# Optimization experiments

Hardware: AMD Instinct MI355X
Metric: run time of the kernel (lower is better)

Reference implementation:

```python
import jax, jax.numpy as jnp
import numpy as np

N, D_IN, F = 65536, 512, 256
E = 524288
BATCH, K1 = 32, 200
BN_EPS = 1e-5


def setup_inputs() -> dict:
    key = jax.random.key(0)
    ks = iter(jax.random.split(key, 64))

    def nrm(shape, s=0.05):
        return jax.random.normal(next(ks), shape, jnp.float32) * s

    inp = {
        "feat": jax.random.normal(next(ks), (N, D_IN), jnp.float32),
        "A": jax.random.randint(next(ks), (2, E), 0, N, dtype=jnp.int32),
        "h1id": jax.random.randint(next(ks), (BATCH * K1,), 0, N // BATCH, dtype=jnp.int32),
        "batch": BATCH,
    }
    dims = [(D_IN, F), (F, F), (F, F), (F, F)]
    for i, (di, do) in enumerate(dims, 1):
        inp[f"eps{i}"] = jnp.zeros((), jnp.float32)          # GINConv train_eps, init 0
        inp[f"w{i}a"] = nrm((di, do)); inp[f"b{i}a"] = jnp.zeros((do,), jnp.float32)
        inp[f"w{i}b"] = nrm((do, do)); inp[f"b{i}b"] = jnp.zeros((do,), jnp.float32)
        inp[f"g{i}"] = jnp.ones((do,), jnp.float32)          # BN gamma
        inp[f"be{i}"] = jnp.zeros((do,), jnp.float32)        # BN beta
        inp[f"m{i}"] = nrm((do,))                            # BN running mean
        inp[f"v{i}"] = jax.random.uniform(next(ks), (do,), jnp.float32, 0.5, 1.5)  # BN running var
    inp["wc1"] = nrm((F, F)); inp["bc1"] = jnp.zeros((F,), jnp.float32)
    inp["pa"] = jnp.full((F,), 0.25, jnp.float32)            # PReLU per-channel slope
    inp["wc2"] = nrm((F, 2)); inp["bc2"] = jnp.zeros((2,), jnp.float32)
    return inp


def _gin_conv(x, src, dst, eps, wa, ba, wb, bb, g, be, m, v):
    # sum aggregation over in-edges: aggr[i] = sum_{(j->i)} x[j]
    aggr = jax.ops.segment_sum(x[src], dst, num_segments=N)
    h = (1.0 + eps) * x + aggr
    h = jax.nn.relu(h @ wa + ba) @ wb + bb
    # BatchNorm1d in eval mode (running stats)
    return (h - m) * jax.lax.rsqrt(v + BN_EPS) * g + be


def _forward(feat, A, h1id, batch,
             eps1, w1a, b1a, w1b, b1b, g1, be1, m1, v1,
             eps2, w2a, b2a, w2b, b2b, g2, be2, m2, v2,
             eps3, w3a, b3a, w3b, b3b, g3, be3, m3, v3,
             eps4, w4a, b4a, w4b, b4b, g4, be4, m4, v4,
             wc1, bc1, pa, wc2, bc2):
    src, dst = A[0], A[1]
    h = jax.nn.relu(_gin_conv(feat, src, dst, eps1, w1a, b1a, w1b, b1b, g1, be1, m1, v1))
    h = jax.nn.relu(_gin_conv(h, src, dst, eps2, w2a, b2a, w2b, b2b, g2, be2, m2, v2))
    h = jax.nn.relu(_gin_conv(h, src, dst, eps3, w3a, b3a, w3b, b3b, g3, be3, m3, v3))
    h = _gin_conv(h, src, dst, eps4, w4a, b4a, w4b, b4b, g4, be4, m4, v4)
    score = h.reshape(batch, -1, F)                      # [B, n_per_graph, F]
    idx = h1id.reshape(batch, K1)
    edge_feat = jnp.take_along_axis(score, idx[:, :, None], axis=1)  # [B, K1, F]
    ef = edge_feat.reshape(-1, F)
    hc = ef @ wc1 + bc1
    hc = jnp.where(hc > 0, hc, pa * hc)                  # PReLU(256)
    return hc @ wc2 + bc2                                # [B*K1, 2]


def reference(feat, A, h1id, batch,
              eps1, w1a, b1a, w1b, b1b, g1, be1, m1, v1,
              eps2, w2a, b2a, w2b, b2b, g2, be2, m2, v2,
              eps3, w3a, b3a, w3b, b3b, g3, be3, m3, v3,
              eps4, w4a, b4a, w4b, b4b, g4, be4, m4, v4,
              wc1, bc1, pa, wc2, bc2):
    return _forward(feat, A, h1id, batch,
                    eps1, w1a, b1a, w1b, b1b, g1, be1, m1, v1,
                    eps2, w2a, b2a, w2b, b2b, g2, be2, m2, v2,
                    eps3, w3a, b3a, w3b, b3b, g3, be3, m3, v3,
                    eps4, w4a, b4a, w4b, b4b, g4, be4, m4, v4,
                    wc1, bc1, pa, wc2, bc2)
```

## Files before the change

kernel.cpp:

```cpp
#include <hip/hip_runtime.h>

typedef unsigned short u16;
typedef unsigned int   u32;
typedef __bf16  bf16x8 __attribute__((ext_vector_type(8)));
typedef float   f32x4  __attribute__((ext_vector_type(4)));

#define NN 65536
#define NE 524288
#define FD 256

typedef const __attribute__((address_space(1))) void* gas_p;
typedef __attribute__((address_space(3))) void* las_p;
#define GLDS16(g, l) __builtin_amdgcn_global_load_lds((gas_p)(const void*)(g), (las_p)(void*)(l), 16, 0, 0)

__device__ __forceinline__ u16 f2bf(float f){
  u32 u = __float_as_uint(f);
  u += 0x7fffu + ((u >> 16) & 1u);
  return (u16)(u >> 16);
}
__device__ __forceinline__ float bf2f(u32 lo16){
  return __uint_as_float(lo16 << 16);
}

__global__ __launch_bounds__(256) void prep_k(
    const float* __restrict__ w1a, const float* __restrict__ w1b,
    const float* __restrict__ w2a, const float* __restrict__ w2b,
    const float* __restrict__ w3a, const float* __restrict__ w3b,
    const float* __restrict__ w4a, const float* __restrict__ w4b,
    const float* __restrict__ wc1, u16* __restrict__ wT)
{
  int idx = blockIdx.x * 256 + threadIdx.x;
  const float* src; int base, K, local;
  if (idx < 131072){ src = w1a; base = 0; K = 512; local = idx; }
  else {
    local = idx - 131072;
    int j = local >> 16;
    local &= 65535;
    K = 256;
    base = 131072 + j * 65536;
    switch (j){
      case 0: src = w1b; break;
      case 1: src = w2a; break;
      case 2: src = w2b; break;
      case 3: src = w3a; break;
      case 4: src = w3b; break;
      case 5: src = w4a; break;
      case 6: src = w4b; break;
      default: src = wc1; break;
    }
  }
  int n = local & 255;
  int k = local >> 8;
  wT[base + n * K + k] = f2bf(src[k * 256 + n]);
}

__global__ __launch_bounds__(256) void hist_k(const int* __restrict__ dst, int* __restrict__ deg){
  int e = blockIdx.x * 256 + threadIdx.x;
  atomicAdd(&deg[dst[e]], 1);
}

__global__ __launch_bounds__(1024) void scan_k(const int* __restrict__ deg, int* __restrict__ rs){
  __shared__ int part[1024];
  int t = threadIdx.x;
  int base = t * 64;
  int sum = 0;
  for (int i = 0; i < 64; ++i) sum += deg[base + i];
  part[t] = sum;
  __syncthreads();
  for (int off = 1; off < 1024; off <<= 1){
    int v = 0;
    if (t >= off) v = part[t - off];
    __syncthreads();
    part[t] += v;
    __syncthreads();
  }
  int run = part[t] - sum;
  for (int i = 0; i < 64; ++i){ rs[base + i] = run; run += deg[base + i]; }
  if (t == 1023) rs[65536] = part[1023];
}

__global__ __launch_bounds__(256) void scat_k(
    const int* __restrict__ src, const int* __restrict__ dst,
    const int* __restrict__ rs, int* __restrict__ cursor, int* __restrict__ csr)
{
  int e = blockIdx.x * 256 + threadIdx.x;
  int d = dst[e];
  int pos = atomicAdd(&cursor[d], 1);
  csr[rs[d] + pos] = src[e];
}

template<int AF32, int MODE, int RELU, int K>
__global__ __launch_bounds__(256) void gemm_k(
    const void* __restrict__ Ap, const u16* __restrict__ Bt,
    u16* __restrict__ C,
    const float* __restrict__ p0, const float* __restrict__ p1,
    const float* __restrict__ p2, const float* __restrict__ p3,
    const float* __restrict__ p4)
{
  __shared__ u16 lds[128 * 136];
  u16* As = lds;
  u16* Bs = lds + 8192;
  const int t    = threadIdx.x;
  const int lane = t & 63;
  const int w    = t >> 6;
  const int wm   = w & 1;
  const int wn   = w >> 1;
  const int m0   = blockIdx.x * 128;
  const int n0   = blockIdx.y * 128;
  const int mrow = lane & 15;
  const int quad = lane >> 4;

  f32x4 acc[4][4];
  const f32x4 zero = {0.f, 0.f, 0.f, 0.f};
  #pragma unroll
  for (int i = 0; i < 4; ++i)
    #pragma unroll
    for (int j = 0; j < 4; ++j) acc[i][j] = zero;

  const u16* Ab = (const u16*)Ap;
  const float* Af = (const float*)Ap;

  for (int k0 = 0; k0 < K; k0 += 64){
    if (AF32){
      #pragma unroll
      for (int i = 0; i < 4; ++i){
        int p   = i * 256 + t;
        int row = p >> 3;
        int ch  = (p & 7) ^ (row & 7);
        const float* s = Af + (size_t)(m0 + row) * K + k0 + ch * 8;
        float4 x0 = *(const float4*)s;
        float4 x1 = *(const float4*)(s + 4);
        union { uint4 q; u16 h[8]; } u;
        u.h[0] = f2bf(x0.x); u.h[1] = f2bf(x0.y); u.h[2] = f2bf(x0.z); u.h[3] = f2bf(x0.w);
        u.h[4] = f2bf(x1.x); u.h[5] = f2bf(x1.y); u.h[6] = f2bf(x1.z); u.h[7] = f2bf(x1.w);
        *(uint4*)&As[p * 8] = u.q;
      }
    } else {
      #pragma unroll
      for (int i = 0; i < 4; ++i){
        int p   = i * 256 + t;
        int row = p >> 3;
        int ch  = (p & 7) ^ (row & 7);
        GLDS16(Ab + (size_t)(m0 + row) * K + k0 + ch * 8, &As[p * 8]);
      }
    }
    #pragma unroll
    for (int i = 0; i < 4; ++i){
      int p   = i * 256 + t;
      int row = p >> 3;
      int ch  = (p & 7) ^ (row & 7);
      GLDS16(Bt + (size_t)(n0 + row) * K + k0 + ch * 8, &Bs[p * 8]);
    }
    __syncthreads();
    #pragma unroll
    for (int ks = 0; ks < 2; ++ks){
      bf16x8 af[4], bq[4];
      #pragma unroll
      for (int mi = 0; mi < 4; ++mi){
        int r  = wm * 64 + mi * 16 + mrow;
        int ch = (quad + ks * 4) ^ (r & 7);
        af[mi] = *(const bf16x8*)&As[(r * 8 + ch) * 8];
      }
      #pragma unroll
      for (int ni = 0; ni < 4; ++ni){
        int r  = wn * 64 + ni * 16 + mrow;
        int ch = (quad + ks * 4) ^ (r & 7);
        bq[ni] = *(const bf16x8*)&Bs[(r * 8 + ch) * 8];
      }
      #pragma unroll
      for (int mi = 0; mi < 4; ++mi)
        #pragma unroll
        for (int ni = 0; ni < 4; ++ni)
          acc[mi][ni] = __builtin_amdgcn_mfma_f32_16x16x32_bf16(af[mi], bq[ni], acc[mi][ni], 0, 0, 0);
    }
    __syncthreads();
  }

  #pragma unroll
  for (int ni = 0; ni < 4; ++ni){
    int c  = wn * 64 + ni * 16 + mrow;
    int gc = n0 + c;
    float scale = 1.f, shift = 0.f, slope = 0.f;
    if (MODE == 1){
      float s = p0[gc] * rsqrtf(p3[gc] + 1e-5f);
      scale = s;
      shift = (p4[gc] - p2[gc]) * s + p1[gc];
    }
    if (MODE == 2){ shift = p0[gc]; slope = p1[gc]; }
    #pragma unroll
    for (int mi = 0; mi < 4; ++mi){
      int rbase = wm * 64 + mi * 16 + quad * 4;
      #pragma unroll
      for (int reg = 0; reg < 4; ++reg){
        float v = acc[mi][ni][reg];
        if (MODE == 1){
          v = v * scale + shift;
          if (RELU) v = fmaxf(v, 0.f);
        }
        if (MODE == 2){
          v += shift;
          v = v > 0.f ? v : slope * v;
        }
        lds[(rbase + reg) * 136 + c] = f2bf(v);
      }
    }
  }
  __syncthreads();
  #pragma unroll
  for (int i = 0; i < 8; ++i){
    int p  = i * 256 + t;
    int r  = p >> 4;
    int ch = p & 15;
    uint4 q = *(const uint4*)&lds[r * 136 + ch * 8];
    *(uint4*)&C[(size_t)(m0 + r) * 256 + n0 + ch * 8] = q;
  }
}

__global__ __launch_bounds__(256) void agg_k(
    const u16* __restrict__ y, const int* __restrict__ rs, const int* __restrict__ csr,
    const float* __restrict__ epsp, const float* __restrict__ bias, u16* __restrict__ tout)
{
  int node = blockIdx.x * 4 + (threadIdx.x >> 6);
  int lane = threadIdx.x & 63;
  int f0 = lane * 4;
  float e1 = 1.0f + epsp[0];
  int s0 = rs[node], s1 = rs[node + 1];
  float a0 = 0.f, a1 = 0.f, a2 = 0.f, a3 = 0.f;
  for (int e = s0; e < s1; ++e){
    int s = csr[e];
    uint2 v = *(const uint2*)(y + (size_t)s * 256 + f0);
    a0 += bf2f(v.x & 0xffffu);
    a1 += bf2f(v.x >> 16);
    a2 += bf2f(v.y & 0xffffu);
    a3 += bf2f(v.y >> 16);
  }
  uint2 own = *(const uint2*)(y + (size_t)node * 256 + f0);
  float4 bv = *(const float4*)(bias + f0);
  float r0 = fmaxf(e1 * bf2f(own.x & 0xffffu) + a0 + bv.x, 0.f);
  float r1 = fmaxf(e1 * bf2f(own.x >> 16)     + a1 + bv.y, 0.f);
  float r2 = fmaxf(e1 * bf2f(own.y & 0xffffu) + a2 + bv.z, 0.f);
  float r3 = fmaxf(e1 * bf2f(own.y >> 16)     + a3 + bv.w, 0.f);
  uint2 o;
  o.x = (u32)f2bf(r0) | ((u32)f2bf(r1) << 16);
  o.y = (u32)f2bf(r2) | ((u32)f2bf(r3) << 16);
  *(uint2*)(tout + (size_t)node * 256 + f0) = o;
}

__global__ __launch_bounds__(256) void agg_g(
    const u16* __restrict__ y, const int* __restrict__ rs, const int* __restrict__ csr,
    const float* __restrict__ epsp, const float* __restrict__ bias,
    const int* __restrict__ gidx, u16* __restrict__ tout)
{
  int gr   = blockIdx.x * 4 + (threadIdx.x >> 6);
  int node = (gr / 200) * 2048 + gidx[gr];
  int lane = threadIdx.x & 63;
  int f0 = lane * 4;
  float e1 = 1.0f + epsp[0];
  int s0 = rs[node], s1 = rs[node + 1];
  float a0 = 0.f, a1 = 0.f, a2 = 0.f, a3 = 0.f;
  for (int e = s0; e < s1; ++e){
    int s = csr[e];
    uint2 v = *(const uint2*)(y + (size_t)s * 256 + f0);
    a0 += bf2f(v.x & 0xffffu);
    a1 += bf2f(v.x >> 16);
    a2 += bf2f(v.y & 0xffffu);
    a3 += bf2f(v.y >> 16);
  }
  uint2 own = *(const uint2*)(y + (size_t)node * 256 + f0);
  float4 bv = *(const float4*)(bias + f0);
  float r0 = fmaxf(e1 * bf2f(own.x & 0xffffu) + a0 + bv.x, 0.f);
  float r1 = fmaxf(e1 * bf2f(own.x >> 16)     + a1 + bv.y, 0.f);
  float r2 = fmaxf(e1 * bf2f(own.y & 0xffffu) + a2 + bv.z, 0.f);
  float r3 = fmaxf(e1 * bf2f(own.y >> 16)     + a3 + bv.w, 0.f);
  uint2 o;
  o.x = (u32)f2bf(r0) | ((u32)f2bf(r1) << 16);
  o.y = (u32)f2bf(r2) | ((u32)f2bf(r3) << 16);
  *(uint2*)(tout + (size_t)gr * 256 + f0) = o;
}

__global__ __launch_bounds__(256) void head_k(
    const u16* __restrict__ hc, const float* __restrict__ wc2,
    const float* __restrict__ bc2, float* __restrict__ out)
{
  int row  = blockIdx.x * 4 + (threadIdx.x >> 6);
  int lane = threadIdx.x & 63;
  int f0   = lane * 4;
  uint2 hv = *(const uint2*)(hc + (size_t)row * 256 + f0);
  float h0 = bf2f(hv.x & 0xffffu), h1 = bf2f(hv.x >> 16);
  float h2 = bf2f(hv.y & 0xffffu), h3 = bf2f(hv.y >> 16);
  float4 wa = *(const float4*)(wc2 + f0 * 2);
  float4 wb = *(const float4*)(wc2 + f0 * 2 + 4);
  float acc0 = h0 * wa.x + h1 * wa.z + h2 * wb.x + h3 * wb.z;
  float acc1 = h0 * wa.y + h1 * wa.w + h2 * wb.y + h3 * wb.w;
  #pragma unroll
  for (int off = 32; off > 0; off >>= 1){
    acc0 += __shfl_xor(acc0, off);
    acc1 += __shfl_xor(acc1, off);
  }
  if (lane == 0){
    out[row * 2]     = acc0 + bc2[0];
    out[row * 2 + 1] = acc1 + bc2[1];
  }
}

extern "C" void kernel_launch(void* const* d_in, const int* in_sizes, int n_in,
                              void* d_out, int out_size, void* d_ws, size_t ws_size,
                              hipStream_t stream)
{
  const float* feat = (const float*)d_in[0];
  const int*   A    = (const int*)d_in[1];
  const int*   h1id = (const int*)d_in[2];
  const float* eps[4] = {(const float*)d_in[4],  (const float*)d_in[13], (const float*)d_in[22], (const float*)d_in[31]};
  const float* wa [4] = {(const float*)d_in[5],  (const float*)d_in[14], (const float*)d_in[23], (const float*)d_in[32]};
  const float* ba [4] = {(const float*)d_in[6],  (const float*)d_in[15], (const float*)d_in[24], (const float*)d_in[33]};
  const float* wb [4] = {(const float*)d_in[7],  (const float*)d_in[16], (const float*)d_in[25], (const float*)d_in[34]};
  const float* bb [4] = {(const float*)d_in[8],  (const float*)d_in[17], (const float*)d_in[26], (const float*)d_in[35]};
  const float* g  [4] = {(const float*)d_in[9],  (const float*)d_in[18], (const float*)d_in[27], (const float*)d_in[36]};
  const float* be [4] = {(const float*)d_in[10], (const float*)d_in[19], (const float*)d_in[28], (const float*)d_in[37]};
  const float* m  [4] = {(const float*)d_in[11], (const float*)d_in[20], (const float*)d_in[29], (const float*)d_in[38]};
  const float* v  [4] = {(const float*)d_in[12], (const float*)d_in[21], (const float*)d_in[30], (const float*)d_in[39]};
  const float* wc1 = (const float*)d_in[40];
  const float* bc1 = (const float*)d_in[41];
  const float* pa  = (const float*)d_in[42];
  const float* wc2 = (const float*)d_in[43];
  const float* bc2 = (const float*)d_in[44];

  char* ws = (char*)d_ws;
  u16* wT     = (u16*)(ws + 0);
  int* deg    = (int*)(ws + 1310720);
  int* rs     = (int*)(ws + 1572864);
  int* cursor = (int*)(ws + 1835264);
  int* csr    = (int*)(ws + 2097408);
  u16* ybuf   = (u16*)(ws + 4194560);
  u16* tbuf   = (u16*)(ws + 37748992);
  u16* hbuf   = (u16*)(ws + 71303424);
  u16* h4     = (u16*)(ws + 104857856);
  u16* hc     = (u16*)(ws + 108134656);

  u16* w1aT = wT;
  u16* w1bT = wT + 131072;
  u16* w2aT = wT + 196608;
  u16* w2bT = wT + 262144;
  u16* w3aT = wT + 327680;
  u16* w3bT = wT + 393216;
  u16* w4aT = wT + 458752;
  u16* w4bT = wT + 524288;
  u16* wc1T = wT + 589824;

  hipMemsetAsync(deg, 0, 65536 * 4, stream);
  hipMemsetAsync(cursor, 0, 65536 * 4, stream);
  prep_k<<<2560, 256, 0, stream>>>(wa[0], wb[0], wa[1], wb[1], wa[2], wb[2], wa[3], wb[3], wc1, wT);
  hist_k<<<NE / 256, 256, 0, stream>>>(A + NE, deg);
  scan_k<<<1, 1024, 0, stream>>>(deg, rs);
  scat_k<<<NE / 256, 256, 0, stream>>>(A, A + NE, rs, cursor, csr);

  const u16* waT[4] = {w1aT, w2aT, w3aT, w4aT};
  const u16* wbT[4] = {w1bT, w2bT, w3bT, w4bT};

  dim3 gBig(512, 2), gSmall(50, 2);

  gemm_k<1,0,0,512><<<gBig, 256, 0, stream>>>(feat, waT[0], ybuf,
      nullptr, nullptr, nullptr, nullptr, nullptr);
  agg_k<<<NN / 4, 256, 0, stream>>>(ybuf, rs, csr, eps[0], ba[0], tbuf);
  gemm_k<0,1,1,256><<<gBig, 256, 0, stream>>>(tbuf, wbT[0], hbuf,
      g[0], be[0], m[0], v[0], bb[0]);

  for (int l = 1; l <= 2; ++l){
    gemm_k<0,0,0,256><<<gBig, 256, 0, stream>>>(hbuf, waT[l], ybuf,
        nullptr, nullptr, nullptr, nullptr, nullptr);
    agg_k<<<NN / 4, 256, 0, stream>>>(ybuf, rs, csr, eps[l], ba[l], tbuf);
    gemm_k<0,1,1,256><<<gBig, 256, 0, stream>>>(tbuf, wbT[l], hbuf,
        g[l], be[l], m[l], v[l], bb[l]);
  }

  gemm_k<0,0,0,256><<<gBig, 256, 0, stream>>>(hbuf, waT[3], ybuf,
      nullptr, nullptr, nullptr, nullptr, nullptr);
  agg_g<<<1600, 256, 0, stream>>>(ybuf, rs, csr, eps[3], ba[3], h1id, tbuf);
  gemm_k<0,1,0,256><<<gSmall, 256, 0, stream>>>(tbuf, wbT[3], h4,
      g[3], be[3], m[3], v[3], bb[3]);

  gemm_k<0,2,0,256><<<gSmall, 256, 0, stream>>>(h4, wc1T, hc,
      bc1, pa, nullptr, nullptr, nullptr);
  head_k<<<1600, 256, 0, stream>>>(hc, wc2, bc2, (float*)d_out);

  (void)in_sizes; (void)n_in; (void)out_size; (void)ws_size;
}
```

Measured before the change: 723.0 us.

## Compute full 256-column output tile per block with 512 threads

Each GEMM block now covers all 256 output columns for its 128 rows using 8 waves. Previously two blocks per row tile each loaded and converted the same A rows, so A traffic (including the fp32-to-bf16 conversion in layer 1) is now paid once. Output stores use nontemporal hints. The cost is more LDS per block (64KB) and fewer, larger blocks, which may lower occupancy.

Result: no change. 734.8 us (+1.6%).

```diff
diff --git a/kernel.cpp b/kernel.cpp
--- a/kernel.cpp
+++ b/kernel.cpp
@@ -4,6 +4,7 @@
 typedef unsigned int   u32;
 typedef __bf16  bf16x8 __attribute__((ext_vector_type(8)));
 typedef float   f32x4  __attribute__((ext_vector_type(4)));
+typedef u32     u32x4  __attribute__((ext_vector_type(4)));
 
 #define NN 65536
 #define NE 524288
@@ -90,14 +91,14 @@
 }
 
 template<int AF32, int MODE, int RELU, int K>
-__global__ __launch_bounds__(256) void gemm_k(
+__global__ __launch_bounds__(512) void gemm_k(
     const void* __restrict__ Ap, const u16* __restrict__ Bt,
     u16* __restrict__ C,
     const float* __restrict__ p0, const float* __restrict__ p1,
     const float* __restrict__ p2, const float* __restrict__ p3,
     const float* __restrict__ p4)
 {
-  __shared__ u16 lds[128 * 136];
+  __shared__ u16 lds[32768];
   u16* As = lds;
   u16* Bs = lds + 8192;
   const int t    = threadIdx.x;
@@ -106,7 +107,6 @@
   const int wm   = w & 1;
   const int wn   = w >> 1;
   const int m0   = blockIdx.x * 128;
-  const int n0   = blockIdx.y * 128;
   const int mrow = lane & 15;
   const int quad = lane >> 4;
 
@@ -123,22 +123,22 @@
   for (int k0 = 0; k0 < K; k0 += 64){
     if (AF32){
       #pragma unroll
-      for (int i = 0; i < 4; ++i){
-        int p   = i * 256 + t;
+      for (int i = 0; i < 2; ++i){
+        int p   = i * 512 + t;
         int row = p >> 3;
-        int ch  = (p & 7) ^ (row & 7);
-        const float* s = Af + (size_t)(m0 + row) * K + k0 + ch * 8;
+        const float* s = Af + (size_t)(m0 + row) * K + k0 + (p & 7) * 8;
         float4 x0 = *(const float4*)s;
         float4 x1 = *(const float4*)(s + 4);
-        union { uint4 q; u16 h[8]; } u;
+        union { u32x4 q; u16 h[8]; } u;
         u.h[0] = f2bf(x0.x); u.h[1] = f2bf(x0.y); u.h[2] = f2bf(x0.z); u.h[3] = f2bf(x0.w);
         u.h[4] = f2bf(x1.x); u.h[5] = f2bf(x1.y); u.h[6] = f2bf(x1.z); u.h[7] = f2bf(x1.w);
-        *(uint4*)&As[p * 8] = u.q;
+        int dst = (p & ~7) | ((p & 7) ^ (row & 7));
+        *(u32x4*)&As[dst * 8] = u.q;
       }
     } else {
       #pragma unroll
-      for (int i = 0; i < 4; ++i){
-        int p   = i * 256 + t;
+      for (int i = 0; i < 2; ++i){
+        int p   = i * 512 + t;
         int row = p >> 3;
         int ch  = (p & 7) ^ (row & 7);
         GLDS16(Ab + (size_t)(m0 + row) * K + k0 + ch * 8, &As[p * 8]);
@@ -146,10 +146,10 @@
     }
     #pragma unroll
     for (int i = 0; i < 4; ++i){
-      int p   = i * 256 + t;
+      int p   = i * 512 + t;
       int row = p >> 3;
       int ch  = (p & 7) ^ (row & 7);
-      GLDS16(Bt + (size_t)(n0 + row) * K + k0 + ch * 8, &Bs[p * 8]);
+      GLDS16(Bt + (size_t)row * K + k0 + ch * 8, &Bs[p * 8]);
     }
     __syncthreads();
     #pragma unroll
@@ -163,9 +163,9 @@
       }
       #pragma unroll
       for (int ni = 0; ni < 4; ++ni){
-        int r  = wn * 64 + ni * 16 + mrow;
-        int ch = (quad + ks * 4) ^ (r & 7);
-        bq[ni] = *(const bf16x8*)&Bs[(r * 8 + ch) * 8];
+        int rb = wn * 64 + ni * 16 + mrow;
+        int ch = (quad + ks * 4) ^ (rb & 7);
+        bq[ni] = *(const bf16x8*)&Bs[(rb * 8 + ch) * 8];
       }
       #pragma unroll
       for (int mi = 0; mi < 4; ++mi)
@@ -179,14 +179,13 @@
   #pragma unroll
   for (int ni = 0; ni < 4; ++ni){
     int c  = wn * 64 + ni * 16 + mrow;
-    int gc = n0 + c;
     float scale = 1.f, shift = 0.f, slope = 0.f;
     if (MODE == 1){
-      float s = p0[gc] * rsqrtf(p3[gc] + 1e-5f);
+      float s = p0[c] * rsqrtf(p3[c] + 1e-5f);
       scale = s;
-      shift = (p4[gc] - p2[gc]) * s + p1[gc];
-    }
-    if (MODE == 2){ shift = p0[gc]; slope = p1[gc]; }
+      shift = (p4[c] - p2[c]) * s + p1[c];
+    }
+    if (MODE == 2){ shift = p0[c]; slope = p1[c]; }
     #pragma unroll
     for (int mi = 0; mi < 4; ++mi){
       int rbase = wm * 64 + mi * 16 + quad * 4;
@@ -201,18 +200,18 @@
           v += shift;
           v = v > 0.f ? v : slope * v;
         }
-        lds[(rbase + reg) * 136 + c] = f2bf(v);
+        lds[(rbase + reg) * 256 + c] = f2bf(v);
       }
     }
   }
   __syncthreads();
   #pragma unroll
   for (int i = 0; i < 8; ++i){
-    int p  = i * 256 + t;
-    int r  = p >> 4;
-    int ch = p & 15;
-    uint4 q = *(const uint4*)&lds[r * 136 + ch * 8];
-    *(uint4*)&C[(size_t)(m0 + r) * 256 + n0 + ch * 8] = q;
+    int p  = i * 512 + t;
+    int r  = p >> 5;
+    int ch = p & 31;
+    u32x4 q = *(const u32x4*)&lds[r * 256 + ch * 8];
+    __builtin_nontemporal_store(q, (u32x4*)&C[(size_t)(m0 + r) * 256 + ch * 8]);
   }
 }
 
@@ -357,29 +356,27 @@
   const u16* waT[4] = {w1aT, w2aT, w3aT, w4aT};
   const u16* wbT[4] = {w1bT, w2bT, w3bT, w4bT};
 
-  dim3 gBig(512, 2), gSmall(50, 2);
-
-  gemm_k<1,0,0,512><<<gBig, 256, 0, stream>>>(feat, waT[0], ybuf,
+  gemm_k<1,0,0,512><<<512, 512, 0, stream>>>(feat, waT[0], ybuf,
       nullptr, nullptr, nullptr, nullptr, nullptr);
   agg_k<<<NN / 4, 256, 0, stream>>>(ybuf, rs, csr, eps[0], ba[0], tbuf);
-  gemm_k<0,1,1,256><<<gBig, 256, 0, stream>>>(tbuf, wbT[0], hbuf,
+  gemm_k<0,1,1,256><<<512, 512, 0, stream>>>(tbuf, wbT[0], hbuf,
       g[0], be[0], m[0], v[0], bb[0]);
 
   for (int l = 1; l <= 2; ++l){
-    gemm_k<0,0,0,256><<<gBig, 256, 0, stream>>>(hbuf, waT[l], ybuf,
+    gemm_k<0,0,0,256><<<512, 512, 0, stream>>>(hbuf, waT[l], ybuf,
         nullptr, nullptr, nullptr, nullptr, nullptr);
     agg_k<<<NN / 4, 256, 0, stream>>>(ybuf, rs, csr, eps[l], ba[l], tbuf);
-    gemm_k<0,1,1,256><<<gBig, 256, 0, stream>>>(tbuf, wbT[l], hbuf,
+    gemm_k<0,1,1,256><<<512, 512, 0, stream>>>(tbuf, wbT[l], hbuf,
         g[l], be[l], m[l], v[l], bb[l]);
   }
 
-  gemm_k<0,0,0,256><<<gBig, 256, 0, stream>>>(hbuf, waT[3], ybuf,
+  gemm_k<0,0,0,256><<<512, 512, 0, stream>>>(hbuf, waT[3], ybuf,
       nullptr, nullptr, nullptr, nullptr, nullptr);
   agg_g<<<1600, 256, 0, stream>>>(ybuf, rs, csr, eps[3], ba[3], h1id, tbuf);
-  gemm_k<0,1,0,256><<<gSmall, 256, 0, stream>>>(tbuf, wbT[3], h4,
+  gemm_k<0,1,0,256><<<50, 512, 0, stream>>>(tbuf, wbT[3], h4,
       g[3], be[3], m[3], v[3], bb[3]);
 
-  gemm_k<0,2,0,256><<<gSmall, 256, 0, stream>>>(h4, wc1T, hc,
+  gemm_k<0,2,0,256><<<50, 512, 0, stream>>>(h4, wc1T, hc,
       bc1, pa, nullptr, nullptr, nullptr);
   head_k<<<1600, 256, 0, stream>>>(hc, wc2, bc2, (float*)d_out);
 
```
